# Kernel optimization log

Measured on AMD Instinct MI355X. Metric: run time of the kernel, lower is better.

Reference implementation:

```python
import jax, jax.numpy as jnp
import numpy as np

N_EMBD = 1024
N_HEAD = 16
HEAD_DIM = N_EMBD // N_HEAD


def _linear_params(key, fan_in, fan_out):
    kw, kb = jax.random.split(key)
    bound = 1.0 / np.sqrt(fan_in)
    W = jax.random.uniform(kw, (fan_out, fan_in), minval=-bound, maxval=bound, dtype=jnp.float32)
    b = jax.random.uniform(kb, (fan_out,), minval=-bound, maxval=bound, dtype=jnp.float32)
    return W, b


def setup_inputs() -> dict:
    key = jax.random.key(0)
    ks = jax.random.split(key, 7)
    B, T, C = 4, 2048, N_EMBD
    k = jax.random.normal(ks[0], (B, T, C), dtype=jnp.float32)
    q = jax.random.normal(ks[1], (B, T, C), dtype=jnp.float32)
    v = jax.random.normal(ks[2], (B, T, C), dtype=jnp.float32)
    Wk, bk = _linear_params(ks[3], C, C)
    Wq, bq = _linear_params(ks[4], C, C)
    Wv, bv = _linear_params(ks[5], C, C)
    Wo, bo = _linear_params(ks[6], C, C)
    return {"k": k, "q": q, "v": v, "Wk": Wk, "bk": bk, "Wq": Wq, "bq": bq,
            "Wv": Wv, "bv": bv, "Wo": Wo, "bo": bo}


def reference(k, q, v, Wk, bk, Wq, bq, Wv, bv, Wo, bo):
    B, T, C = k.shape
    H, CH = N_HEAD, C // N_HEAD
    # projections (nn.Linear: x @ W.T + b), split heads -> [b, h, t, ch]
    keys = (k @ Wk.T + bk).reshape(B, T, H, CH).transpose(0, 2, 1, 3)
    queries = (q @ Wq.T + bq).reshape(B, T, H, CH).transpose(0, 2, 1, 3)
    values = (v @ Wv.T + bv).reshape(B, T, H, CH).transpose(0, 2, 1, 3)
    # [b, h, t, t] scores, scaled before softmax as in the original
    att = jnp.einsum('bhqd,bhkd->bhqk', queries, keys)
    att = jax.nn.softmax(att * (CH ** -0.5), axis=-1)
    out = jnp.einsum('bhqk,bhkd->bhqd', att, values)
    out = out.transpose(0, 2, 1, 3).reshape(B, T, C)
    return out @ Wo.T + bo
```

## Files before the change

kernel.cpp:

```cpp
#include <hip/hip_runtime.h>


typedef short bf8 __attribute__((ext_vector_type(8)));
typedef float f4 __attribute__((ext_vector_type(4)));
typedef float f16v __attribute__((ext_vector_type(16)));
typedef unsigned short u16;

#define AS1 __attribute__((address_space(1)))
#define AS3 __attribute__((address_space(3)))

__device__ __forceinline__ u16 f2b(float f) {
  unsigned u = __builtin_bit_cast(unsigned, f);
  u += 0x7FFFu + ((u >> 16) & 1u);
  return (u16)(u >> 16);
}

__device__ __forceinline__ unsigned cvtpk(float lo, float hi) {
  unsigned r;
  asm("v_cvt_pk_bf16_f32 %0, %1, %2" : "=v"(r) : "v"(lo), "v"(hi));
  return r;
}

__device__ __forceinline__ void swap32(unsigned& a, unsigned& b) {
  asm("v_permlane32_swap_b32 %0, %1" : "+v"(a), "+v"(b));
}

__global__ void cvt4_kernel(const float* __restrict__ a, const float* __restrict__ b,
                            const float* __restrict__ c, const float* __restrict__ d,
                            u16* __restrict__ out) {
  int i = blockIdx.x * blockDim.x + threadIdx.x;
  const int sel = i >> 18, off = i & 0x3FFFF;
  const float* src = sel == 0 ? a : sel == 1 ? b : sel == 2 ? c : d;
  float4 f = ((const float4*)src)[off];
  ushort4 o;
  o.x = f2b(f.x); o.y = f2b(f.y); o.z = f2b(f.z); o.w = f2b(f.w);
  ((ushort4*)out)[i] = o;
}

template<int MODE>
__device__ __forceinline__ void gemm_epilogue(
    f4 (&acc)[4][4], const float* __restrict__ bias, void* __restrict__ Cout,
    int N, float scale, int m0, int n0, int wm, int wn, int lr, int lg)
{
  if (MODE == 0) {
    float bv[4];
    #pragma unroll
    for (int j = 0; j < 4; ++j) bv[j] = bias[n0 + wn + j * 16 + lr];
    float* C = (float*)Cout;
    #pragma unroll
    for (int i = 0; i < 4; ++i)
      #pragma unroll
      for (int j = 0; j < 4; ++j) {
        const int col = n0 + wn + j * 16 + lr;
        #pragma unroll
        for (int r = 0; r < 4; ++r) {
          const int row = m0 + wm + i * 16 + lg * 4 + r;
          C[(size_t)row * N + col] = acc[i][j][r] + bv[j];
        }
      }
  } else if (MODE == 1) {
    float bv[4];
    #pragma unroll
    for (int j = 0; j < 4; ++j) bv[j] = bias[n0 + wn + j * 16 + lr];
    u16* C = (u16*)Cout;
    #pragma unroll
    for (int i = 0; i < 4; ++i)
      #pragma unroll
      for (int j = 0; j < 4; ++j) {
        const int col = n0 + wn + j * 16 + lr;
        const int h = col >> 6, ch = col & 63;
        #pragma unroll
        for (int r = 0; r < 4; ++r) {
          const int row = m0 + wm + i * 16 + lg * 4 + r;
          const int b = row >> 11, t = row & 2047;
          C[((size_t)(b * 16 + h) * 2048 + t) * 64 + ch] = f2b((acc[i][j][r] + bv[j]) * scale);
        }
      }
  } else {
    u16* C = (u16*)Cout;
    #pragma unroll
    for (int i = 0; i < 4; ++i)
      #pragma unroll
      for (int r = 0; r < 4; ++r) {
        const int nch = m0 + wm + i * 16 + lg * 4 + r;
        const float br = bias[nch];
        const int h = nch >> 6, ch = nch & 63;
        #pragma unroll
        for (int j = 0; j < 4; ++j) {
          const int tok = n0 + wn + j * 16 + lr;
          const int b = tok >> 11, t = tok & 2047;
          C[((size_t)((b * 16 + h) * 64 + ch) << 11) + t] = f2b(acc[i][j][r] + br);
        }
      }
  }
}

template<int MODE, int ACTB>
__device__ __forceinline__ void gemm_fp_body(
    u16* __restrict__ actT, u16* __restrict__ wT,
    const float* __restrict__ act, const u16* __restrict__ Wt,
    const float* __restrict__ bias, void* __restrict__ Cout,
    int N, int K, float scale, int m0, int n0)
{
  const int tid = threadIdx.x, lane = tid & 63, w = tid >> 6;
  const int wm = (w >> 1) << 6, wn = (w & 1) << 6;
  const int lr = lane & 15, lg = lane >> 4;
  const int arow0 = (ACTB ? n0 : m0);
  const int wrow0 = (ACTB ? m0 : n0);

  f4 acc[4][4] = {};
  float4 ta[8];

  #define W_GLDS(buf, karg)                                                     \
    do {                                                                        \
      const int k_ = (karg);                                                    \
      u16* dst = wT + ((buf) << 13);                                            \
      _Pragma("unroll")                                                         \
      for (int q = 0; q < 4; ++q) {                                             \
        const int c = (w << 8) + (q << 6) + lane;                               \
        const int row = c >> 3, sw = ((c & 7) ^ (row & 7)) << 3;                \
        __builtin_amdgcn_global_load_lds(                                       \
            (const AS1 void*)(Wt + (size_t)(wrow0 + row) * K + k_ + sw),        \
            (AS3 void*)(dst + (((w << 2) + q) << 9)), 16, 0, 0);                \
      }                                                                         \
    } while (0)

  #define ACT_LOAD(karg)                                                        \
    do {                                                                        \
      const int k_ = (karg);                                                    \
      _Pragma("unroll")                                                         \
      for (int q = 0; q < 4; ++q) {                                             \
        const int c = (w << 8) + (q << 6) + lane;                               \
        const int row = c >> 3, col = (c & 7) << 3;                             \
        const float* s = act + (size_t)(arow0 + row) * K + k_ + col;            \
        ta[2 * q] = *(const float4*)s;                                          \
        ta[2 * q + 1] = *(const float4*)(s + 4);                                \
      }                                                                         \
    } while (0)

  #define ACT_WRITE(buf)                                                        \
    do {                                                                        \
      u16* dst = actT + ((buf) << 13);                                          \
      _Pragma("unroll")                                                         \
      for (int q = 0; q < 4; ++q) {                                             \
        const int c = (w << 8) + (q << 6) + lane;                               \
        const int row = c >> 3;                                                 \
        uint4 pk;                                                               \
        pk.x = cvtpk(ta[2 * q].x, ta[2 * q].y);                                 \
        pk.y = cvtpk(ta[2 * q].z, ta[2 * q].w);                                 \
        pk.z = cvtpk(ta[2 * q + 1].x, ta[2 * q + 1].y);                         \
        pk.w = cvtpk(ta[2 * q + 1].z, ta[2 * q + 1].w);                         \
        *(uint4*)(dst + (row << 6) + (((c & 7) ^ (row & 7)) << 3)) = pk;        \
      }                                                                         \
    } while (0)

  W_GLDS(0, 0);
  ACT_LOAD(0);
  ACT_WRITE(0);
  ACT_LOAD(64);
  asm volatile("s_waitcnt lgkmcnt(0)" ::: "memory");

  const int NKT = K >> 6;
  for (int kt = 0; kt < NKT; ++kt) {
    const int cur = kt & 1;
    if (kt > 0) {
      if (kt + 1 < NKT) asm volatile("s_waitcnt vmcnt(8)" ::: "memory");
      else              asm volatile("s_waitcnt vmcnt(0)" ::: "memory");
    }
    __builtin_amdgcn_s_barrier();
    __builtin_amdgcn_sched_barrier(0);

    if (kt + 1 < NKT) W_GLDS(cur ^ 1, (kt + 1) << 6);

    const u16* aC = actT + (cur << 13);
    const u16* wC = wT + (cur << 13);
    #pragma unroll
    for (int ks = 0; ks < 2; ++ks) {
      bf8 af[4], bfr[4];
      #pragma unroll
      for (int i = 0; i < 4; ++i) {
        const int ra = wm + i * 16 + lr;
        const int rb = wn + i * 16 + lr;
        const u16* aSrc = ACTB ? wC : aC;
        const u16* bSrc = ACTB ? aC : wC;
        af[i]  = *(const bf8*)(aSrc + (ra << 6) + ((((ks << 2) + lg) ^ (ra & 7)) << 3));
        bfr[i] = *(const bf8*)(bSrc + (rb << 6) + ((((ks << 2) + lg) ^ (rb & 7)) << 3));
      }
      __builtin_amdgcn_s_setprio(1);
      #pragma unroll
      for (int i = 0; i < 4; ++i)
        #pragma unroll
        for (int j = 0; j < 4; ++j)
          acc[i][j] = __builtin_amdgcn_mfma_f32_16x16x32_bf16(af[i], bfr[j], acc[i][j], 0, 0, 0);
      __builtin_amdgcn_s_setprio(0);
    }

    if (kt + 1 < NKT) {
      ACT_WRITE(cur ^ 1);
      if (kt + 2 < NKT) ACT_LOAD((kt + 2) << 6);
    }
    asm volatile("s_waitcnt lgkmcnt(0)" ::: "memory");
  }
  #undef W_GLDS
  #undef ACT_LOAD
  #undef ACT_WRITE

  gemm_epilogue<MODE>(acc, bias, Cout, N, scale, m0, n0, wm, wn, lr, lg);
}

__global__ __launch_bounds__(256, 2)
void proj_qkv(const float* __restrict__ q_in, const float* __restrict__ k_in,
              const float* __restrict__ v_in,
              const u16* __restrict__ Wq, const u16* __restrict__ Wk,
              const u16* __restrict__ Wv,
              const float* __restrict__ bq, const float* __restrict__ bk,
              const float* __restrict__ bv,
              u16* __restrict__ Qp, u16* __restrict__ Kp, u16* __restrict__ Vt,
              float qscale)
{
  __shared__ __align__(16) u16 pool[32768];
  u16* const actT = pool;
  u16* const wT   = pool + 16384;

  const int cpx = gridDim.x >> 3;
  const int bid = (blockIdx.x & 7) * cpx + (blockIdx.x >> 3);
  const int which = bid >> 9, sub = bid & 511;

  if (which < 2) {
    gemm_fp_body<1, 0>(actT, wT,
                       which ? k_in : q_in,
                       which ? Wk : Wq,
                       which ? bk : bq,
                       which ? (void*)Kp : (void*)Qp,
                       1024, 1024, which ? 1.f : qscale,
                       (sub >> 3) << 7, (sub & 7) << 7);
  } else {
    gemm_fp_body<2, 1>(actT, wT, v_in, Wv, bv, (void*)Vt,
                       8192, 1024, 1.f, (sub & 7) << 7, (sub >> 3) << 7);
  }
}

__global__ __launch_bounds__(256, 2)
void gemm_out(const u16* __restrict__ A, const u16* __restrict__ B,
              const float* __restrict__ bias, float* __restrict__ C)
{
  __shared__ __align__(16) u16 pool[32768];
  u16* const aT = pool;
  u16* const bT = pool + 16384;

  const int cpx = gridDim.x >> 3;
  const int bid = (blockIdx.x & 7) * cpx + (blockIdx.x >> 3);
  const int m0 = (bid >> 3) << 7, n0 = (bid & 7) << 7;
  const int tid = threadIdx.x, lane = tid & 63, w = tid >> 6;
  const int wm = (w >> 1) << 6, wn = (w & 1) << 6;
  const int lr = lane & 15, lg = lane >> 4;
  const int K = 1024;

  f4 acc[4][4] = {};

  #pragma unroll
  for (int q = 0; q < 4; ++q) {
    const int c = (w << 8) + (q << 6) + lane;
    const int row = c >> 3, sw = ((c & 7) ^ (row & 7)) << 3;
    __builtin_amdgcn_global_load_lds(
        (const AS1 void*)(A + (size_t)(m0 + row) * K + sw),
        (AS3 void*)(aT + (((w << 2) + q) << 9)), 16, 0, 0);
    __builtin_amdgcn_global_load_lds(
        (const AS1 void*)(B + (size_t)(n0 + row) * K + sw),
        (AS3 void*)(bT + (((w << 2) + q) << 9)), 16, 0, 0);
  }
  __syncthreads();

  for (int kt = 0; kt < 16; ++kt) {
    const int cur = kt & 1;
    const u16* aC = aT + (cur << 13);
    const u16* bC = bT + (cur << 13);
    if (kt + 1 < 16) {
      u16* aN = aT + ((cur ^ 1) << 13);
      u16* bN = bT + ((cur ^ 1) << 13);
      const int k1 = (kt + 1) << 6;
      #pragma unroll
      for (int q = 0; q < 4; ++q) {
        const int c = (w << 8) + (q << 6) + lane;
        const int row = c >> 3, sw = ((c & 7) ^ (row & 7)) << 3;
        __builtin_amdgcn_global_load_lds(
            (const AS1 void*)(A + (size_t)(m0 + row) * K + k1 + sw),
            (AS3 void*)(aN + (((w << 2) + q) << 9)), 16, 0, 0);
        __builtin_amdgcn_global_load_lds(
            (const AS1 void*)(B + (size_t)(n0 + row) * K + k1 + sw),
            (AS3 void*)(bN + (((w << 2) + q) << 9)), 16, 0, 0);
      }
    }
    #pragma unroll
    for (int ks = 0; ks < 2; ++ks) {
      bf8 af[4], bfr[4];
      #pragma unroll
      for (int i = 0; i < 4; ++i) {
        const int ra = wm + i * 16 + lr;
        const int rb = wn + i * 16 + lr;
        af[i]  = *(const bf8*)(aC + (ra << 6) + ((((ks << 2) + lg) ^ (ra & 7)) << 3));
        bfr[i] = *(const bf8*)(bC + (rb << 6) + ((((ks << 2) + lg) ^ (rb & 7)) << 3));
      }
      __builtin_amdgcn_s_setprio(1);
      #pragma unroll
      for (int i = 0; i < 4; ++i)
        #pragma unroll
        for (int j = 0; j < 4; ++j)
          acc[i][j] = __builtin_amdgcn_mfma_f32_16x16x32_bf16(af[i], bfr[j], acc[i][j], 0, 0, 0);
      __builtin_amdgcn_s_setprio(0);
    }
    __syncthreads();
  }

  gemm_epilogue<0>(acc, bias, (void*)C, 1024, 1.f, m0, n0, wm, wn, lr, lg);
}

__global__ __launch_bounds__(256, 3)
void attn_kernel(const u16* __restrict__ Qp, const u16* __restrict__ Kp,
                 const u16* __restrict__ VT, u16* __restrict__ Ob)
{
  __shared__ __align__(16) u16 pool[24576];
  u16* const ktb = pool;
  u16* const vtb = pool + 12288;

  const int flat = blockIdx.x;
  const int xcd = flat & 7, idx = flat >> 3;
  const int bh = (xcd << 3) + (idx >> 4);
  const int tq0 = (idx & 15) << 7;

  const int tid = threadIdx.x, lane = tid & 63, w = tid >> 6;
  const int ql = lane & 31, hi = lane >> 5;
  const size_t hoff = (size_t)bh * (2048 * 64);
  const u16* Kh = Kp + hoff;
  const u16* Vh = VT + hoff;

  bf8 qf[4];
  {
    const u16* qp_ = Qp + hoff + (size_t)(tq0 + w * 32 + ql) * 64 + hi * 8;
    #pragma unroll
    for (int ks = 0; ks < 4; ++ks) qf[ks] = *(const bf8*)(qp_ + 16 * ks);
  }

  f16v o0 = {}, o1 = {};
  float lrun = 0.f;

  const int c0i = (w << 7) + lane;
  const int c1i = c0i + 64;
  const int sr0 = c0i >> 3, ss0 = ((c0i & 7) ^ (sr0 & 7)) << 3;
  const int sr1 = c1i >> 3, ss1 = ((c1i & 7) ^ (sr1 & 7)) << 3;
  const int sd0 = (w << 10);
  const int sd1 = (w << 10) + 512;

  #define STAGE(buf, t0)                                                          \
    do {                                                                           \
      __builtin_amdgcn_global_load_lds((const AS1 void*)(Kh + (size_t)((t0) + sr0) * 64 + ss0), \
                                       (AS3 void*)(ktb + (buf) * 4096 + sd0), 16, 0, 0);  \
      __builtin_amdgcn_global_load_lds((const AS1 void*)(Kh + (size_t)((t0) + sr1) * 64 + ss1), \
                                       (AS3 void*)(ktb + (buf) * 4096 + sd1), 16, 0, 0);  \
      __builtin_amdgcn_global_load_lds((const AS1 void*)(Vh + (size_t)sr0 * 2048 + (t0) + ss0), \
                                       (AS3 void*)(vtb + (buf) * 4096 + sd0), 16, 0, 0);  \
      __builtin_amdgcn_global_load_lds((const AS1 void*)(Vh + (size_t)sr1 * 2048 + (t0) + ss1), \
                                       (AS3 void*)(vtb + (buf) * 4096 + sd1), 16, 0, 0);  \
    } while (0)

  STAGE(0, 0);
  STAGE(1, 64);

  const int xq = ql & 7;
  int bc = 0;
  for (int it = 0; it < 32; ++it) {
    if (it < 31) asm volatile("s_waitcnt vmcnt(4)" ::: "memory");
    else         asm volatile("s_waitcnt vmcnt(0)" ::: "memory");
    __builtin_amdgcn_s_barrier();
    __builtin_amdgcn_sched_barrier(0);

    if (it + 2 < 32) {
      const int bs = bc ? bc - 1 : 2;
      STAGE(bs, (it + 2) << 6);
    }

    const u16* kb = ktb + bc * 4096;
    const u16* vb = vtb + bc * 4096;

    f16v s0 = {}, s1 = {};
    #pragma unroll
    for (int ks = 0; ks < 4; ++ks) {
      bf8 kf0 = *(const bf8*)(kb + (ql << 6) + ((((ks << 1) + hi) ^ xq) << 3));
      bf8 kf1 = *(const bf8*)(kb + ((32 + ql) << 6) + ((((ks << 1) + hi) ^ xq) << 3));
      __builtin_amdgcn_s_setprio(1);
      s0 = __builtin_amdgcn_mfma_f32_32x32x16_bf16(kf0, qf[ks], s0, 0, 0, 0);
      s1 = __builtin_amdgcn_mfma_f32_32x32x16_bf16(kf1, qf[ks], s1, 0, 0, 0);
      __builtin_amdgcn_s_setprio(0);
    }

    bf8 vf0[4], vf1[4];
    #pragma unroll
    for (int ks = 0; ks < 4; ++ks) {
      vf0[ks] = *(const bf8*)(vb + (ql << 6) + ((((ks << 1) + hi) ^ xq) << 3));
      vf1[ks] = *(const bf8*)(vb + ((32 + ql) << 6) + ((((ks << 1) + hi) ^ xq) << 3));
    }

    float rs = 0.f;

    {
      unsigned wpk[8];
      #pragma unroll
      for (int i = 0; i < 8; ++i) {
        float e0 = __builtin_amdgcn_exp2f(s0[2 * i]);
        float e1 = __builtin_amdgcn_exp2f(s0[2 * i + 1]);
        rs += e0 + e1;
        wpk[i] = cvtpk(e0, e1);
      }
      swap32(wpk[0], wpk[2]); swap32(wpk[1], wpk[3]);
      swap32(wpk[4], wpk[6]); swap32(wpk[5], wpk[7]);
      bf8 pf0 = __builtin_bit_cast(bf8, make_uint4(wpk[0], wpk[1], wpk[2], wpk[3]));
      bf8 pf1 = __builtin_bit_cast(bf8, make_uint4(wpk[4], wpk[5], wpk[6], wpk[7]));
      __builtin_amdgcn_s_setprio(1);
      o0 = __builtin_amdgcn_mfma_f32_32x32x16_bf16(vf0[0], pf0, o0, 0, 0, 0);
      o1 = __builtin_amdgcn_mfma_f32_32x32x16_bf16(vf1[0], pf0, o1, 0, 0, 0);
      o0 = __builtin_amdgcn_mfma_f32_32x32x16_bf16(vf0[1], pf1, o0, 0, 0, 0);
      o1 = __builtin_amdgcn_mfma_f32_32x32x16_bf16(vf1[1], pf1, o1, 0, 0, 0);
      __builtin_amdgcn_s_setprio(0);
    }

    {
      unsigned wpk[8];
      #pragma unroll
      for (int i = 0; i < 8; ++i) {
        float e0 = __builtin_amdgcn_exp2f(s1[2 * i]);
        float e1 = __builtin_amdgcn_exp2f(s1[2 * i + 1]);
        rs += e0 + e1;
        wpk[i] = cvtpk(e0, e1);
      }
      swap32(wpk[0], wpk[2]); swap32(wpk[1], wpk[3]);
      swap32(wpk[4], wpk[6]); swap32(wpk[5], wpk[7]);
      bf8 pf2 = __builtin_bit_cast(bf8, make_uint4(wpk[0], wpk[1], wpk[2], wpk[3]));
      bf8 pf3 = __builtin_bit_cast(bf8, make_uint4(wpk[4], wpk[5], wpk[6], wpk[7]));
      __builtin_amdgcn_s_setprio(1);
      o0 = __builtin_amdgcn_mfma_f32_32x32x16_bf16(vf0[2], pf2, o0, 0, 0, 0);
      o1 = __builtin_amdgcn_mfma_f32_32x32x16_bf16(vf1[2], pf2, o1, 0, 0, 0);
      o0 = __builtin_amdgcn_mfma_f32_32x32x16_bf16(vf0[3], pf3, o0, 0, 0, 0);
      o1 = __builtin_amdgcn_mfma_f32_32x32x16_bf16(vf1[3], pf3, o1, 0, 0, 0);
      __builtin_amdgcn_s_setprio(0);
    }

    lrun += rs;
    bc = bc + 1 < 3 ? bc + 1 : 0;
  }
  #undef STAGE

  const float linv = 1.f / (lrun + __shfl_xor(lrun, 32));

  __syncthreads();
  u16* const ot = pool;
  const int orow = w * 32 + ql;
  #pragma unroll
  for (int c = 0; c < 2; ++c) {
    const f16v& o = c ? o1 : o0;
    #pragma unroll
    for (int g = 0; g < 4; ++g) {
      uint2 pk;
      pk.x = cvtpk(o[4 * g + 0] * linv, o[4 * g + 1] * linv);
      pk.y = cvtpk(o[4 * g + 2] * linv, o[4 * g + 3] * linv);
      *(uint2*)(ot + orow * 72 + 32 * c + 8 * g + 4 * hi) = pk;
    }
  }
  __syncthreads();

  const int b = bh >> 4, h = bh & 15;
  const int row = tid >> 1, seg = tid & 1;
  const u16* src = ot + row * 72 + seg * 32;
  u16* dst = Ob + ((size_t)(b * 2048 + tq0 + row) * 16 + h) * 64 + seg * 32;
  #pragma unroll
  for (int kk = 0; kk < 4; ++kk)
    *(uint4*)(dst + 8 * kk) = *(const uint4*)(src + 8 * kk);
}

extern "C" void kernel_launch(void* const* d_in, const int* in_sizes, int n_in,
                              void* d_out, int out_size, void* d_ws, size_t ws_size,
                              hipStream_t stream) {
  (void)in_sizes; (void)n_in; (void)out_size; (void)ws_size;
  const float* k_in = (const float*)d_in[0];
  const float* q_in = (const float*)d_in[1];
  const float* v_in = (const float*)d_in[2];
  const float* Wk = (const float*)d_in[3]; const float* bk = (const float*)d_in[4];
  const float* Wq = (const float*)d_in[5]; const float* bq = (const float*)d_in[6];
  const float* Wv = (const float*)d_in[7]; const float* bv = (const float*)d_in[8];
  const float* Wo = (const float*)d_in[9]; const float* bo = (const float*)d_in[10];
  float* out = (float*)d_out;

  char* ws = (char*)d_ws;
  const size_t SZ_ACT = (size_t)8192 * 1024 * 2;
  const size_t SZ_W   = (size_t)1024 * 1024 * 2;
  u16* Oc  = (u16*)(ws);
  u16* Qp  = (u16*)(ws + 1 * SZ_ACT);
  u16* Kp  = (u16*)(ws + 2 * SZ_ACT);
  u16* Vt  = (u16*)(ws + 3 * SZ_ACT);
  u16* Wqb = (u16*)(ws + 4 * SZ_ACT);
  u16* Wkb = (u16*)(ws + 4 * SZ_ACT + SZ_W);
  u16* Wvb = (u16*)(ws + 4 * SZ_ACT + 2 * SZ_W);
  u16* Wob = (u16*)(ws + 4 * SZ_ACT + 3 * SZ_W);

  cvt4_kernel<<<4096, 256, 0, stream>>>(Wq, Wk, Wv, Wo, Wqb);

  const float c0 = 0.125f * 1.4426950408889634f;

  proj_qkv<<<1536, 256, 0, stream>>>(q_in, k_in, v_in, Wqb, Wkb, Wvb,
                                     bq, bk, bv, Qp, Kp, Vt, c0);

  attn_kernel<<<1024, 256, 0, stream>>>(Qp, Kp, Vt, Oc);

  gemm_out<<<512, 256, 0, stream>>>(Oc, Wob, bo, out);
}
```

Before: 179.1 us.

## Use 512-thread blocks with 8 waves in QKV projection GEMM

The fused QKV projection kernel now launches 512 threads per block, with 8 waves each computing a 64x32 sub-tile instead of 4 waves computing 64x64. Each thread loads and converts half as much activation and weight data per k-step, and the vmcnt wait is adjusted to match. The aim is more waves in flight to hide global-load and fp32-to-bf16 conversion latency, with fewer accumulator registers per thread. In exchange, each wave issues fewer MFMAs per LDS fragment load, which lowers per-wave data reuse. The launch bound claims 4 blocks per CU, which the 64KB LDS per block may not allow.

After: 178.0 us, median of 2. No clear change (-0.6%).

```diff
diff --git a/kernel.cpp b/kernel.cpp
--- a/kernel.cpp
+++ b/kernel.cpp
@@ -37,36 +37,144 @@
   ((ushort4*)out)[i] = o;
 }
 
-template<int MODE>
-__device__ __forceinline__ void gemm_epilogue(
-    f4 (&acc)[4][4], const float* __restrict__ bias, void* __restrict__ Cout,
-    int N, float scale, int m0, int n0, int wm, int wn, int lr, int lg)
+__device__ __forceinline__ void gemm_epilogue44(
+    f4 (&acc)[4][4], const float* __restrict__ bias, float* __restrict__ C,
+    int N, int m0, int n0, int wm, int wn, int lr, int lg)
 {
-  if (MODE == 0) {
-    float bv[4];
-    #pragma unroll
-    for (int j = 0; j < 4; ++j) bv[j] = bias[n0 + wn + j * 16 + lr];
-    float* C = (float*)Cout;
+  float bv[4];
+  #pragma unroll
+  for (int j = 0; j < 4; ++j) bv[j] = bias[n0 + wn + j * 16 + lr];
+  #pragma unroll
+  for (int i = 0; i < 4; ++i)
+    #pragma unroll
+    for (int j = 0; j < 4; ++j) {
+      const int col = n0 + wn + j * 16 + lr;
+      #pragma unroll
+      for (int r = 0; r < 4; ++r) {
+        const int row = m0 + wm + i * 16 + lg * 4 + r;
+        C[(size_t)row * N + col] = acc[i][j][r] + bv[j];
+      }
+    }
+}
+
+template<int MODE, int ACTB>
+__device__ __forceinline__ void gemm_fp_body8(
+    u16* __restrict__ actT, u16* __restrict__ wT,
+    const float* __restrict__ act, const u16* __restrict__ Wt,
+    const float* __restrict__ bias, void* __restrict__ Cout,
+    int N, int K, float scale, int m0, int n0)
+{
+  const int tid = threadIdx.x, lane = tid & 63, w = tid >> 6;
+  const int wm = (w >> 2) << 6;
+  const int wn = (w & 3) << 5;
+  const int lr = lane & 15, lg = lane >> 4;
+  const int arow0 = (ACTB ? n0 : m0);
+  const int wrow0 = (ACTB ? m0 : n0);
+
+  f4 acc[4][2] = {};
+  float4 ta[4];
+
+  const int r0 = tid >> 3, x0 = tid & 7;
+  const int r1 = r0 + 64;
+  const int wsw0 = (x0 ^ (r0 & 7)) << 3;
+  const int wsw1 = (x0 ^ (r1 & 7)) << 3;
+
+  #define W_GLDS(buf, karg)                                                     \
+    do {                                                                        \
+      const int k_ = (karg);                                                    \
+      u16* dst = wT + ((buf) << 13);                                            \
+      __builtin_amdgcn_global_load_lds(                                         \
+          (const AS1 void*)(Wt + (size_t)(wrow0 + r0) * K + k_ + wsw0),         \
+          (AS3 void*)(dst + (w << 9)), 16, 0, 0);                               \
+      __builtin_amdgcn_global_load_lds(                                         \
+          (const AS1 void*)(Wt + (size_t)(wrow0 + r1) * K + k_ + wsw1),         \
+          (AS3 void*)(dst + 4096 + (w << 9)), 16, 0, 0);                        \
+    } while (0)
+
+  #define ACT_LOAD(karg)                                                        \
+    do {                                                                        \
+      const int k_ = (karg);                                                    \
+      const float* s0 = act + (size_t)(arow0 + r0) * K + k_ + (x0 << 3);        \
+      const float* s1 = act + (size_t)(arow0 + r1) * K + k_ + (x0 << 3);        \
+      ta[0] = *(const float4*)s0; ta[1] = *(const float4*)(s0 + 4);             \
+      ta[2] = *(const float4*)s1; ta[3] = *(const float4*)(s1 + 4);             \
+    } while (0)
+
+  #define ACT_WRITE(buf)                                                        \
+    do {                                                                        \
+      u16* dst = actT + ((buf) << 13);                                          \
+      uint4 pk0, pk1;                                                           \
+      pk0.x = cvtpk(ta[0].x, ta[0].y); pk0.y = cvtpk(ta[0].z, ta[0].w);         \
+      pk0.z = cvtpk(ta[1].x, ta[1].y); pk0.w = cvtpk(ta[1].z, ta[1].w);         \
+      pk1.x = cvtpk(ta[2].x, ta[2].y); pk1.y = cvtpk(ta[2].z, ta[2].w);         \
+      pk1.z = cvtpk(ta[3].x, ta[3].y); pk1.w = cvtpk(ta[3].z, ta[3].w);         \
+      *(uint4*)(dst + (r0 << 6) + wsw0) = pk0;                                  \
+      *(uint4*)(dst + (r1 << 6) + wsw1) = pk1;                                  \
+    } while (0)
+
+  W_GLDS(0, 0);
+  ACT_LOAD(0);
+  ACT_WRITE(0);
+  ACT_LOAD(64);
+  asm volatile("s_waitcnt lgkmcnt(0)" ::: "memory");
+
+  const int NKT = K >> 6;
+  for (int kt = 0; kt < NKT; ++kt) {
+    const int cur = kt & 1;
+    if (kt > 0) {
+      if (kt + 1 < NKT) asm volatile("s_waitcnt vmcnt(4)" ::: "memory");
+      else              asm volatile("s_waitcnt vmcnt(0)" ::: "memory");
+    }
+    __builtin_amdgcn_s_barrier();
+    __builtin_amdgcn_sched_barrier(0);
+
+    if (kt + 1 < NKT) W_GLDS(cur ^ 1, (kt + 1) << 6);
+
+    const u16* aC = actT + (cur << 13);
+    const u16* wC = wT + (cur << 13);
+    #pragma unroll
+    for (int ks = 0; ks < 2; ++ks) {
+      const u16* aSrc = ACTB ? wC : aC;
+      const u16* bSrc = ACTB ? aC : wC;
+      bf8 af[4], bfr[2];
+      #pragma unroll
+      for (int i = 0; i < 4; ++i) {
+        const int ra = wm + i * 16 + lr;
+        af[i] = *(const bf8*)(aSrc + (ra << 6) + ((((ks << 2) + lg) ^ (ra & 7)) << 3));
+      }
+      #pragma unroll
+      for (int j = 0; j < 2; ++j) {
+        const int rb = wn + j * 16 + lr;
+        bfr[j] = *(const bf8*)(bSrc + (rb << 6) + ((((ks << 2) + lg) ^ (rb & 7)) << 3));
+      }
+      __builtin_amdgcn_s_setprio(1);
+      #pragma unroll
+      for (int i = 0; i < 4; ++i)
+        #pragma unroll
+        for (int j = 0; j < 2; ++j)
+          acc[i][j] = __builtin_amdgcn_mfma_f32_16x16x32_bf16(af[i], bfr[j], acc[i][j], 0, 0, 0);
+      __builtin_amdgcn_s_setprio(0);
+    }
+
+    if (kt + 1 < NKT) {
+      ACT_WRITE(cur ^ 1);
+      if (kt + 2 < NKT) ACT_LOAD((kt + 2) << 6);
+    }
+    asm volatile("s_waitcnt lgkmcnt(0)" ::: "memory");
+  }
+  #undef W_GLDS
+  #undef ACT_LOAD
+  #undef ACT_WRITE
+
+  if (MODE == 1) {
+    float bv[2];
+    #pragma unroll
+    for (int j = 0; j < 2; ++j) bv[j] = bias[n0 + wn + j * 16 + lr];
+    u16* C = (u16*)Cout;
     #pragma unroll
     for (int i = 0; i < 4; ++i)
       #pragma unroll
-      for (int j = 0; j < 4; ++j) {
-        const int col = n0 + wn + j * 16 + lr;
-        #pragma unroll
-        for (int r = 0; r < 4; ++r) {
-          const int row = m0 + wm + i * 16 + lg * 4 + r;
-          C[(size_t)row * N + col] = acc[i][j][r] + bv[j];
-        }
-      }
-  } else if (MODE == 1) {
-    float bv[4];
-    #pragma unroll
-    for (int j = 0; j < 4; ++j) bv[j] = bias[n0 + wn + j * 16 + lr];
-    u16* C = (u16*)Cout;
-    #pragma unroll
-    for (int i = 0; i < 4; ++i)
-      #pragma unroll
-      for (int j = 0; j < 4; ++j) {
+      for (int j = 0; j < 2; ++j) {
         const int col = n0 + wn + j * 16 + lr;
         const int h = col >> 6, ch = col & 63;
         #pragma unroll
@@ -86,7 +194,7 @@
         const float br = bias[nch];
         const int h = nch >> 6, ch = nch & 63;
         #pragma unroll
-        for (int j = 0; j < 4; ++j) {
+        for (int j = 0; j < 2; ++j) {
           const int tok = n0 + wn + j * 16 + lr;
           const int b = tok >> 11, t = tok & 2047;
           C[((size_t)((b * 16 + h) * 64 + ch) << 11) + t] = f2b(acc[i][j][r] + br);
@@ -95,120 +203,7 @@
   }
 }
 
-template<int MODE, int ACTB>
-__device__ __forceinline__ void gemm_fp_body(
-    u16* __restrict__ actT, u16* __restrict__ wT,
-    const float* __restrict__ act, const u16* __restrict__ Wt,
-    const float* __restrict__ bias, void* __restrict__ Cout,
-    int N, int K, float scale, int m0, int n0)
-{
-  const int tid = threadIdx.x, lane = tid & 63, w = tid >> 6;
-  const int wm = (w >> 1) << 6, wn = (w & 1) << 6;
-  const int lr = lane & 15, lg = lane >> 4;
-  const int arow0 = (ACTB ? n0 : m0);
-  const int wrow0 = (ACTB ? m0 : n0);
-
-  f4 acc[4][4] = {};
-  float4 ta[8];
-
-  #define W_GLDS(buf, karg)                                                     \
-    do {                                                                        \
-      const int k_ = (karg);                                                    \
-      u16* dst = wT + ((buf) << 13);                                            \
-      _Pragma("unroll")                                                         \
-      for (int q = 0; q < 4; ++q) {                                             \
-        const int c = (w << 8) + (q << 6) + lane;                               \
-        const int row = c >> 3, sw = ((c & 7) ^ (row & 7)) << 3;                \
-        __builtin_amdgcn_global_load_lds(                                       \
-            (const AS1 void*)(Wt + (size_t)(wrow0 + row) * K + k_ + sw),        \
-            (AS3 void*)(dst + (((w << 2) + q) << 9)), 16, 0, 0);                \
-      }                                                                         \
-    } while (0)
-
-  #define ACT_LOAD(karg)                                                        \
-    do {                                                                        \
-      const int k_ = (karg);                                                    \
-      _Pragma("unroll")                                                         \
-      for (int q = 0; q < 4; ++q) {                                             \
-        const int c = (w << 8) + (q << 6) + lane;                               \
-        const int row = c >> 3, col = (c & 7) << 3;                             \
-        const float* s = act + (size_t)(arow0 + row) * K + k_ + col;            \
-        ta[2 * q] = *(const float4*)s;                                          \
-        ta[2 * q + 1] = *(const float4*)(s + 4);                                \
-      }                                                                         \
-    } while (0)
-
-  #define ACT_WRITE(buf)                                                        \
-    do {                                                                        \
-      u16* dst = actT + ((buf) << 13);                                          \
-      _Pragma("unroll")                                                         \
-      for (int q = 0; q < 4; ++q) {                                             \
-        const int c = (w << 8) + (q << 6) + lane;                               \
-        const int row = c >> 3;                                                 \
-        uint4 pk;                                                               \
-        pk.x = cvtpk(ta[2 * q].x, ta[2 * q].y);                                 \
-        pk.y = cvtpk(ta[2 * q].z, ta[2 * q].w);                                 \
-        pk.z = cvtpk(ta[2 * q + 1].x, ta[2 * q + 1].y);                         \
-        pk.w = cvtpk(ta[2 * q + 1].z, ta[2 * q + 1].w);                         \
-        *(uint4*)(dst + (row << 6) + (((c & 7) ^ (row & 7)) << 3)) = pk;        \
-      }                                                                         \
-    } while (0)
-
-  W_GLDS(0, 0);
-  ACT_LOAD(0);
-  ACT_WRITE(0);
-  ACT_LOAD(64);
-  asm volatile("s_waitcnt lgkmcnt(0)" ::: "memory");
-
-  const int NKT = K >> 6;
-  for (int kt = 0; kt < NKT; ++kt) {
-    const int cur = kt & 1;
-    if (kt > 0) {
-      if (kt + 1 < NKT) asm volatile("s_waitcnt vmcnt(8)" ::: "memory");
-      else              asm volatile("s_waitcnt vmcnt(0)" ::: "memory");
-    }
-    __builtin_amdgcn_s_barrier();
-    __builtin_amdgcn_sched_barrier(0);
-
-    if (kt + 1 < NKT) W_GLDS(cur ^ 1, (kt + 1) << 6);
-
-    const u16* aC = actT + (cur << 13);
-    const u16* wC = wT + (cur << 13);
-    #pragma unroll
-    for (int ks = 0; ks < 2; ++ks) {
-      bf8 af[4], bfr[4];
-      #pragma unroll
-      for (int i = 0; i < 4; ++i) {
-        const int ra = wm + i * 16 + lr;
-        const int rb = wn + i * 16 + lr;
-        const u16* aSrc = ACTB ? wC : aC;
-        const u16* bSrc = ACTB ? aC : wC;
-        af[i]  = *(const bf8*)(aSrc + (ra << 6) + ((((ks << 2) + lg) ^ (ra & 7)) << 3));
-        bfr[i] = *(const bf8*)(bSrc + (rb << 6) + ((((ks << 2) + lg) ^ (rb & 7)) << 3));
-      }
-      __builtin_amdgcn_s_setprio(1);
-      #pragma unroll
-      for (int i = 0; i < 4; ++i)
-        #pragma unroll
-        for (int j = 0; j < 4; ++j)
-          acc[i][j] = __builtin_amdgcn_mfma_f32_16x16x32_bf16(af[i], bfr[j], acc[i][j], 0, 0, 0);
-      __builtin_amdgcn_s_setprio(0);
-    }
-
-    if (kt + 1 < NKT) {
-      ACT_WRITE(cur ^ 1);
-      if (kt + 2 < NKT) ACT_LOAD((kt + 2) << 6);
-    }
-    asm volatile("s_waitcnt lgkmcnt(0)" ::: "memory");
-  }
-  #undef W_GLDS
-  #undef ACT_LOAD
-  #undef ACT_WRITE
-
-  gemm_epilogue<MODE>(acc, bias, Cout, N, scale, m0, n0, wm, wn, lr, lg);
-}
-
-__global__ __launch_bounds__(256, 2)
+__global__ __launch_bounds__(512, 4)
 void proj_qkv(const float* __restrict__ q_in, const float* __restrict__ k_in,
               const float* __restrict__ v_in,
               const u16* __restrict__ Wq, const u16* __restrict__ Wk,
@@ -227,16 +222,16 @@
   const int which = bid >> 9, sub = bid & 511;
 
   if (which < 2) {
-    gemm_fp_body<1, 0>(actT, wT,
-                       which ? k_in : q_in,
-                       which ? Wk : Wq,
-                       which ? bk : bq,
-                       which ? (void*)Kp : (void*)Qp,
-                       1024, 1024, which ? 1.f : qscale,
-                       (sub >> 3) << 7, (sub & 7) << 7);
+    gemm_fp_body8<1, 0>(actT, wT,
+                        which ? k_in : q_in,
+                        which ? Wk : Wq,
+                        which ? bk : bq,
+                        which ? (void*)Kp : (void*)Qp,
+                        1024, 1024, which ? 1.f : qscale,
+                        (sub >> 3) << 7, (sub & 7) << 7);
   } else {
-    gemm_fp_body<2, 1>(actT, wT, v_in, Wv, bv, (void*)Vt,
-                       8192, 1024, 1.f, (sub & 7) << 7, (sub >> 3) << 7);
+    gemm_fp_body8<2, 1>(actT, wT, v_in, Wv, bv, (void*)Vt,
+                        8192, 1024, 1.f, (sub & 7) << 7, (sub >> 3) << 7);
   }
 }
 
@@ -312,7 +307,7 @@
     __syncthreads();
   }
 
-  gemm_epilogue<0>(acc, bias, (void*)C, 1024, 1.f, m0, n0, wm, wn, lr, lg);
+  gemm_epilogue44(acc, bias, C, 1024, m0, n0, wm, wn, lr, lg);
 }
 
 __global__ __launch_bounds__(256, 3)
@@ -505,7 +500,7 @@
 
   const float c0 = 0.125f * 1.4426950408889634f;
 
-  proj_qkv<<<1536, 256, 0, stream>>>(q_in, k_in, v_in, Wqb, Wkb, Wvb,
+  proj_qkv<<<1536, 512, 0, stream>>>(q_in, k_in, v_in, Wqb, Wkb, Wvb,
                                      bq, bk, bv, Qp, Kp, Vt, c0);
 
   attn_kernel<<<1024, 256, 0, stream>>>(Qp, Kp, Vt, Oc);
```
